# Optimization experiments

Measured on AMD Instinct MI355X. Metric: run time of the kernel, lower is better.

## Reference

```python
import jax, jax.numpy as jnp
import numpy as np

DIM = 4096
N_HEADS = 32
N_KV = 8
HD = 128
SW = 4096          # sliding window / cache length
B = 32             # max_batch_size (decode batch)
MAX_SEQ = 8192
START_POS = 4000
CURRENT_POS = 4000

def _nearest_32(n):
    return ((n + 31) // 32) * 32

PADDED_LEN = min(_nearest_32(START_POS + 1), SW)  # 4032

def _rope_tables():
    inv_freq = 1.0 / (10000.0 ** (np.arange(0, HD, 2, dtype=np.float32) / HD))
    t = np.arange(MAX_SEQ, dtype=np.float32)
    freqs = np.outer(t, inv_freq)                       # [MAX_SEQ, HD/2]
    emb = np.concatenate([freqs, freqs], axis=-1)       # [MAX_SEQ, HD]
    return jnp.asarray(np.cos(emb)), jnp.asarray(np.sin(emb))

def rotate_half(u):
    u1, u2 = jnp.split(u, 2, axis=-1)
    return jnp.concatenate([-u2, u1], axis=-1)

def setup_inputs() -> dict:
    key = jax.random.key(0)
    ks = jax.random.split(key, 6)
    cos_cached, sin_cached = _rope_tables()
    return {
        "x": jax.random.normal(ks[0], (1, 1, B, DIM), jnp.float32),
        "wqkv": jax.random.normal(ks[1], (DIM, DIM + 2 * N_KV * HD), jnp.float32) * 0.02,
        "wo": jax.random.normal(ks[2], (DIM, DIM), jnp.float32) * 0.02,
        "cache_k": jax.random.normal(ks[3], (B, N_KV, SW, HD), jnp.float32) * 0.5,
        "cache_v": jax.random.normal(ks[4], (B, N_KV, SW, HD), jnp.float32) * 0.5,
        "cos_cached": cos_cached,
        "sin_cached": sin_cached,
        "attn_mask": jnp.zeros((B, N_HEADS, 1, PADDED_LEN), jnp.float32),
        "start_pos": START_POS,
        "current_pos": CURRENT_POS,
    }

def reference(x, wqkv, wo, cache_k, cache_v, cos_cached, sin_cached, attn_mask,
              start_pos, current_pos):
    group = N_HEADS // N_KV
    padded_len = min(_nearest_32(start_pos + 1), SW)
    scale = 1.0 / jnp.sqrt(jnp.float32(HD))

    # fused QKV projection: x (1,1,B,DIM) @ wqkv -> (B, DIM + 2*N_KV*HD)
    xqkv = x[0, 0] @ wqkv
    q = xqkv[:, :DIM].reshape(B, N_HEADS, HD)
    k = xqkv[:, DIM:DIM + N_KV * HD].reshape(B, N_KV, HD)
    v = xqkv[:, DIM + N_KV * HD:].reshape(B, N_KV, HD)

    # rotary embedding at position start_pos (single decode token)
    cos = cos_cached[start_pos]   # [HD]
    sin = sin_cached[start_pos]
    q = q * cos + rotate_half(q) * sin
    k = k * cos + rotate_half(k) * sin

    # sliding-window KV cache update at current_pos
    cache_k = cache_k.at[:, :, current_pos, :].set(k)
    cache_v = cache_v.at[:, :, current_pos, :].set(v)
    keys = cache_k[:, :, :padded_len, :]     # [B, N_KV, L, HD]
    values = cache_v[:, :, :padded_len, :]

    # grouped attention: q heads grouped by kv head
    qg = q.reshape(B, N_KV, group, HD)
    scores = jnp.einsum('bkgd,bkld->bkgl', qg, keys) * scale
    scores = scores + attn_mask.reshape(B, N_KV, group, padded_len)
    probs = jax.nn.softmax(scores, axis=-1)
    out = jnp.einsum('bkgl,bkld->bkgd', probs, values)   # [B, N_KV, group, HD]

    # concat heads and output projection
    dense = out.reshape(B, DIM) @ wo
    return dense.reshape(1, 1, B, DIM)
```

## Files before the change

### kernel.cpp

```cpp
#include <hip/hip_runtime.h>
#include <hip/hip_bf16.h>

typedef unsigned int u32;
typedef unsigned short u16;

__device__ __forceinline__ u16 f2bf(float f){ u32 x; __builtin_memcpy(&x,&f,4); u32 r=(x+0x7fffu+((x>>16)&1u))>>16; return (u16)r; }
__device__ __forceinline__ float lo2f(u32 u){ u32 x=u<<16; float f; __builtin_memcpy(&f,&x,4); return f; }
__device__ __forceinline__ float hi2f(u32 u){ u32 x=u&0xffff0000u; float f; __builtin_memcpy(&f,&x,4); return f; }

__global__ __launch_bounds__(256) void transpose_x(
    const float* __restrict__ x, float* __restrict__ xt)
{
    __shared__ float ld[32][65];
    const int t = threadIdx.x;
    const int g = blockIdx.x;
    #pragma unroll
    for (int i=0;i<8;++i) {
        const int e = i*256 + t;
        const int b = e >> 6, dd = e & 63;
        ld[b][dd] = x[(size_t)b*4096 + g*64 + dd];
    }
    __syncthreads();
    #pragma unroll
    for (int i=0;i<8;++i) {
        const int e = i*256 + t;
        const int dd = e >> 5, b = e & 31;
        xt[(size_t)(g*64 + dd)*32 + b] = ld[b][dd];
    }
}

__global__ __launch_bounds__(256) void gemm_splitk_t(
    const float* __restrict__ At, const float2* __restrict__ W2,
    float* __restrict__ P, int K, int N, int dps)
{
    const int j2 = blockIdx.x*256 + threadIdx.x;
    const int s = blockIdx.y;
    float acc0[32], acc1[32];
    #pragma unroll
    for (int b=0;b<32;++b){ acc0[b]=0.f; acc1[b]=0.f; }
    const int d0 = s*dps, d1 = d0 + dps;
    const int halfN = N >> 1;
    #pragma unroll 2
    for (int d=d0; d<d1; ++d) {
        const float2 wv = W2[(size_t)d*halfN + j2];
        const float* __restrict__ Ad = At + d*32;
        #pragma unroll
        for (int b=0;b<32;++b) {
            const float av = Ad[b];
            acc0[b] = fmaf(av, wv.x, acc0[b]);
            acc1[b] = fmaf(av, wv.y, acc1[b]);
        }
    }
    float* Pp = P + (size_t)(s*32)*N + 2*j2;
    #pragma unroll
    for (int b=0;b<32;++b)
        *reinterpret_cast<float2*>(Pp + (size_t)b*N) = make_float2(acc0[b], acc1[b]);
}

__global__ __launch_bounds__(256) void qkv_finish(
    const float* __restrict__ P, const float* __restrict__ cosc,
    const float* __restrict__ sinc, const int* __restrict__ spp,
    float* __restrict__ qws, float* __restrict__ kn, float* __restrict__ vn,
    int splits)
{
    __shared__ float sh[256];
    const int t = threadIdx.x;
    const int col = blockIdx.x*256 + t;
    const int b = blockIdx.y;
    float v = 0.f;
    for (int s=0;s<splits;++s) v += P[(size_t)(s*32+b)*6144 + col];
    sh[t] = v;
    __syncthreads();
    if (col < 5120) {
        const int d = col & 127;
        const int pt = (t & ~127) | ((d<64)? d+64 : d-64);
        const float pv = sh[pt];
        const int spos = *spp;
        const float c  = cosc[spos*128 + d];
        const float sn = sinc[spos*128 + d];
        const float rot = (d<64)? -pv : pv;
        const float val = fmaf(v, c, rot*sn);
        if (col < 4096) qws[(size_t)b*4096 + col] = val;
        else            kn[(size_t)b*1024 + (col-4096)] = val;
    } else {
        vn[(size_t)b*1024 + (col-5120)] = v;
    }
}

__global__ __launch_bounds__(1024, 4) void attn_kernel(
    const float* __restrict__ qws, const float* __restrict__ Kc,
    const float* __restrict__ Vc, const float* __restrict__ kn,
    const float* __restrict__ vn, const float* __restrict__ mask,
    const int* __restrict__ curp, float* __restrict__ aout_t,
    const int PL, const int SW)
{
    __shared__ float scoresS[4*4100];
    __shared__ uint2 probsP[4096];
    __shared__ float obuf[16][4][128];
    __shared__ float redm[16][4];
    __shared__ float reds[16][4];

    const int t = threadIdx.x;
    const int lane = t & 63;
    const int w = t >> 6;
    const int b  = blockIdx.x >> 3;
    const int kv = blockIdx.x & 7;
    const int cur = *curp;

    const size_t mat = (size_t)(b*8+kv);
    const float* __restrict__ Kb  = Kc + mat*(size_t)SW*128;
    const float* __restrict__ knr = kn + mat*128;
    const float* __restrict__ qbase = qws + (size_t)(b*32 + kv*4)*128;

    const int l   = lane & 15;
    const int grp = lane >> 4;
    float qv[4][8];
    #pragma unroll
    for (int h=0;h<4;++h)
        #pragma unroll
        for (int j=0;j<8;++j)
            qv[h][j] = qbase[h*128 + l*8 + j];

    const int rpw = PL >> 4;
    const int rb0 = w * rpw;
    for (int g=0; g<rpw; g+=4) {
        const int r = rb0 + g + grp;
        const float* __restrict__ row = (r==cur) ? knr : (Kb + (size_t)r*128);
        const float4 ka = *reinterpret_cast<const float4*>(row + l*8);
        const float4 kb4 = *reinterpret_cast<const float4*>(row + l*8 + 4);
        float kf[8];
        kf[0]=ka.x; kf[1]=ka.y; kf[2]=ka.z; kf[3]=ka.w;
        kf[4]=kb4.x; kf[5]=kb4.y; kf[6]=kb4.z; kf[7]=kb4.w;
        float sc0=0.f, sc1=0.f, sc2=0.f, sc3=0.f;
        #pragma unroll
        for (int j=0;j<8;++j) {
            sc0 = fmaf(qv[0][j], kf[j], sc0);
            sc1 = fmaf(qv[1][j], kf[j], sc1);
            sc2 = fmaf(qv[2][j], kf[j], sc2);
            sc3 = fmaf(qv[3][j], kf[j], sc3);
        }
        #pragma unroll
        for (int off=8; off; off>>=1) {
            sc0 += __shfl_xor(sc0, off, 16);
            sc1 += __shfl_xor(sc1, off, 16);
            sc2 += __shfl_xor(sc2, off, 16);
            sc3 += __shfl_xor(sc3, off, 16);
        }
        if (l < 4) {
            const float v = (l==0)?sc0:(l==1)?sc1:(l==2)?sc2:sc3;
            scoresS[l*4100 + r] = v;
        }
    }
    __syncthreads();

    const float scale = 0.08838834764831845f;
    const size_t mbase = ((size_t)b*32 + (size_t)kv*4)*(size_t)PL;
    float s[4][4];
    #pragma unroll
    for (int i=0;i<4;++i) {
        const int p = i*1024 + t;
        if (p < PL) {
            #pragma unroll
            for (int h=0;h<4;++h) {
                const float mv = mask[mbase + (size_t)h*PL + p];
                s[h][i] = fmaf(scoresS[h*4100 + p], scale, mv);
            }
        } else {
            #pragma unroll
            for (int h=0;h<4;++h) s[h][i] = -3.0e38f;
        }
    }

    float lm[4];
    #pragma unroll
    for (int h=0;h<4;++h)
        lm[h] = fmaxf(fmaxf(s[h][0],s[h][1]), fmaxf(s[h][2],s[h][3]));
    #pragma unroll
    for (int off=1; off<64; off<<=1) {
        #pragma unroll
        for (int h=0;h<4;++h) lm[h] = fmaxf(lm[h], __shfl_xor(lm[h], off, 64));
    }
    if (lane==0) {
        #pragma unroll
        for (int h=0;h<4;++h) redm[w][h] = lm[h];
    }
    __syncthreads();
    float M[4];
    #pragma unroll
    for (int h=0;h<4;++h) {
        float m = redm[0][h];
        #pragma unroll
        for (int ww=1;ww<16;++ww) m = fmaxf(m, redm[ww][h]);
        M[h] = m;
    }

    float ls[4] = {0.f,0.f,0.f,0.f};
    #pragma unroll
    for (int i=0;i<4;++i) {
        #pragma unroll
        for (int h=0;h<4;++h) {
            const float e = __expf(s[h][i] - M[h]);
            s[h][i] = e;
            ls[h] += e;
        }
    }
    #pragma unroll
    for (int off=1; off<64; off<<=1) {
        #pragma unroll
        for (int h=0;h<4;++h) ls[h] += __shfl_xor(ls[h], off, 64);
    }
    if (lane==0) {
        #pragma unroll
        for (int h=0;h<4;++h) reds[w][h] = ls[h];
    }
    __syncthreads();
    float inv[4];
    #pragma unroll
    for (int h=0;h<4;++h) {
        float sm = reds[0][h];
        #pragma unroll
        for (int ww=1;ww<16;++ww) sm += reds[ww][h];
        inv[h] = 1.f / sm;
    }

    #pragma unroll
    for (int i=0;i<4;++i) {
        const int p = i*1024 + t;
        if (p < PL) {
            const u32 plo = (u32)f2bf(s[0][i]*inv[0]) | ((u32)f2bf(s[1][i]*inv[1]) << 16);
            const u32 phi = (u32)f2bf(s[2][i]*inv[2]) | ((u32)f2bf(s[3][i]*inv[3]) << 16);
            probsP[p] = make_uint2(plo, phi);
        }
    }
    __syncthreads();

    const float* __restrict__ Vb  = Vc + mat*(size_t)SW*128;
    const float* __restrict__ vnr = vn + mat*128;
    const int chunk = PL >> 4;
    const int p0 = w*chunk, p1 = p0 + chunk;
    float a0[4] = {0.f,0.f,0.f,0.f}, a1[4] = {0.f,0.f,0.f,0.f};
    #pragma unroll 8
    for (int p=p0; p<p1; ++p) {
        const float* row = (p==cur) ? vnr : (Vb + (size_t)p*128);
        const float2 vv = *reinterpret_cast<const float2*>(row + 2*lane);
        const uint2 pp = probsP[p];
        const float pr0 = lo2f(pp.x), pr1 = hi2f(pp.x);
        const float pr2 = lo2f(pp.y), pr3 = hi2f(pp.y);
        a0[0]=fmaf(pr0,vv.x,a0[0]); a1[0]=fmaf(pr0,vv.y,a1[0]);
        a0[1]=fmaf(pr1,vv.x,a0[1]); a1[1]=fmaf(pr1,vv.y,a1[1]);
        a0[2]=fmaf(pr2,vv.x,a0[2]); a1[2]=fmaf(pr2,vv.y,a1[2]);
        a0[3]=fmaf(pr3,vv.x,a0[3]); a1[3]=fmaf(pr3,vv.y,a1[3]);
    }
    #pragma unroll
    for (int h=0;h<4;++h)
        *reinterpret_cast<float2*>(&obuf[w][h][2*lane]) = make_float2(a0[h], a1[h]);
    __syncthreads();

    if (t < 512) {
        const int h = t >> 7;
        const int d = t & 127;
        float sum = obuf[0][h][d];
        #pragma unroll
        for (int ww=1;ww<16;++ww) sum += obuf[ww][h][d];
        const int col = (kv*4 + h)*128 + d;
        aout_t[(size_t)col*32 + b] = sum;
    }
}

__global__ __launch_bounds__(256) void wo_finish(
    const float* __restrict__ P, float* __restrict__ out, int splits)
{
    const int col = blockIdx.x*256 + threadIdx.x;
    const int b = blockIdx.y;
    float v = 0.f;
    for (int s=0;s<splits;++s) v += P[(size_t)(s*32+b)*4096 + col];
    out[(size_t)b*4096 + col] = v;
}

extern "C" void kernel_launch(void* const* d_in, const int* in_sizes, int n_in,
                              void* d_out, int out_size, void* d_ws, size_t ws_size,
                              hipStream_t stream)
{
    const float* x    = (const float*)d_in[0];
    const float* wqkv = (const float*)d_in[1];
    const float* wo   = (const float*)d_in[2];
    const float* cK   = (const float*)d_in[3];
    const float* cV   = (const float*)d_in[4];
    const float* cosc = (const float*)d_in[5];
    const float* sinc = (const float*)d_in[6];
    const float* mask = (const float*)d_in[7];
    const int* sp   = (const int*)d_in[8];
    const int* cp   = (const int*)d_in[9];

    const int PL = in_sizes[7] / (32*32);
    const int SW = in_sizes[3] / (32*8*128);

    char* ws = (char*)d_ws;
    float* xt    = (float*)(ws);
    float* qws   = (float*)(ws + 524288);
    float* aout_t= (float*)(ws + 2*524288);
    float* kn    = (float*)(ws + 3*524288);
    float* vn    = (float*)(ws + 3*524288 + 131072);
    float* Pbuf  = (float*)(ws + 3*524288 + 2*131072);

    int splits = 64;
    {
        const size_t fixed = 3ull*524288 + 2ull*131072;
        while (splits > 4 && fixed + (size_t)splits*32*6144*4 > ws_size) splits >>= 1;
    }
    const int dps = 4096 / splits;

    transpose_x<<<64, 256, 0, stream>>>(x, xt);
    gemm_splitk_t<<<dim3(12, splits), 256, 0, stream>>>(xt, (const float2*)wqkv, Pbuf, 4096, 6144, dps);
    qkv_finish<<<dim3(24, 32), 256, 0, stream>>>(Pbuf, cosc, sinc, sp, qws, kn, vn, splits);

    attn_kernel<<<256, 1024, 0, stream>>>(qws, cK, cV, kn, vn, mask, cp, aout_t, PL, SW);

    gemm_splitk_t<<<dim3(8, splits), 256, 0, stream>>>(aout_t, (const float2*)wo, Pbuf, 4096, 4096, dps);
    wo_finish<<<dim3(16, 32), 256, 0, stream>>>(Pbuf, (float*)d_out, splits);
}
```

Measured before the change: 305.0 us.

## Split attention over sequence into partial blocks with flash-decoding combine

Replaces the one-block-per-(batch,kv-head) attention kernel with a split-sequence version: each (batch,kv) pair is split into 8 partitions run by 256-thread blocks that write partial outputs plus running max and sum, and a new combine kernel merges them with log-sum-exp rescaling. This raises the block count from 256 to 2048 to better fill the GPU and hide KV-cache load latency. It costs an extra launch and a round trip for the partial results, and the workspace layout assumes a fixed Pbuf size instead of checking ws_size. Probabilities are stored unnormalised in bf16 before the rescale.

```diff
diff --git a/kernel.cpp b/kernel.cpp
--- a/kernel.cpp
+++ b/kernel.cpp
@@ -87,29 +87,31 @@
     }
 }
 
-__global__ __launch_bounds__(1024, 4) void attn_kernel(
+__global__ __launch_bounds__(256, 8) void attn_part(
     const float* __restrict__ qws, const float* __restrict__ Kc,
     const float* __restrict__ Vc, const float* __restrict__ kn,
     const float* __restrict__ vn, const float* __restrict__ mask,
-    const int* __restrict__ curp, float* __restrict__ aout_t,
-    const int PL, const int SW)
-{
-    __shared__ float scoresS[4*4100];
-    __shared__ uint2 probsP[4096];
-    __shared__ float obuf[16][4][128];
-    __shared__ float redm[16][4];
-    __shared__ float reds[16][4];
+    const int* __restrict__ curp, float* __restrict__ partO,
+    float* __restrict__ partML, const int PL, const int SW)
+{
+    __shared__ float scoresS[4*512];
+    __shared__ float obuf[4][4][128];
+    __shared__ float redm[4][4];
+    __shared__ float reds[4][4];
 
     const int t = threadIdx.x;
     const int lane = t & 63;
     const int w = t >> 6;
-    const int b  = blockIdx.x >> 3;
-    const int kv = blockIdx.x & 7;
+    const int mat  = blockIdx.x >> 3;
+    const int part = blockIdx.x & 7;
+    const int b  = mat >> 3;
+    const int kv = mat & 7;
     const int cur = *curp;
-
-    const size_t mat = (size_t)(b*8+kv);
-    const float* __restrict__ Kb  = Kc + mat*(size_t)SW*128;
-    const float* __restrict__ knr = kn + mat*128;
+    const int PS = PL >> 3;
+    const int base = part * PS;
+
+    const float* __restrict__ Kb  = Kc + (size_t)mat*SW*128;
+    const float* __restrict__ knr = kn + (size_t)mat*128;
     const float* __restrict__ qbase = qws + (size_t)(b*32 + kv*4)*128;
 
     const int l   = lane & 15;
@@ -121,49 +123,52 @@
         for (int j=0;j<8;++j)
             qv[h][j] = qbase[h*128 + l*8 + j];
 
-    const int rpw = PL >> 4;
-    const int rb0 = w * rpw;
-    for (int g=0; g<rpw; g+=4) {
-        const int r = rb0 + g + grp;
-        const float* __restrict__ row = (r==cur) ? knr : (Kb + (size_t)r*128);
-        const float4 ka = *reinterpret_cast<const float4*>(row + l*8);
-        const float4 kb4 = *reinterpret_cast<const float4*>(row + l*8 + 4);
-        float kf[8];
-        kf[0]=ka.x; kf[1]=ka.y; kf[2]=ka.z; kf[3]=ka.w;
-        kf[4]=kb4.x; kf[5]=kb4.y; kf[6]=kb4.z; kf[7]=kb4.w;
-        float sc0=0.f, sc1=0.f, sc2=0.f, sc3=0.f;
-        #pragma unroll
-        for (int j=0;j<8;++j) {
-            sc0 = fmaf(qv[0][j], kf[j], sc0);
-            sc1 = fmaf(qv[1][j], kf[j], sc1);
-            sc2 = fmaf(qv[2][j], kf[j], sc2);
-            sc3 = fmaf(qv[3][j], kf[j], sc3);
-        }
-        #pragma unroll
-        for (int off=8; off; off>>=1) {
-            sc0 += __shfl_xor(sc0, off, 16);
-            sc1 += __shfl_xor(sc1, off, 16);
-            sc2 += __shfl_xor(sc2, off, 16);
-            sc3 += __shfl_xor(sc3, off, 16);
-        }
-        if (l < 4) {
-            const float v = (l==0)?sc0:(l==1)?sc1:(l==2)?sc2:sc3;
-            scoresS[l*4100 + r] = v;
+    const int nIter = (PS + 15) >> 4;
+    for (int i=0;i<nIter;++i) {
+        const int rl = i*16 + w*4 + grp;
+        if (rl < PS) {
+            const int r = base + rl;
+            const float* __restrict__ row = (r==cur) ? knr : (Kb + (size_t)r*128);
+            const float4 ka  = *reinterpret_cast<const float4*>(row + l*8);
+            const float4 kb4 = *reinterpret_cast<const float4*>(row + l*8 + 4);
+            float kf[8];
+            kf[0]=ka.x; kf[1]=ka.y; kf[2]=ka.z; kf[3]=ka.w;
+            kf[4]=kb4.x; kf[5]=kb4.y; kf[6]=kb4.z; kf[7]=kb4.w;
+            float sc0=0.f, sc1=0.f, sc2=0.f, sc3=0.f;
+            #pragma unroll
+            for (int j=0;j<8;++j) {
+                sc0 = fmaf(qv[0][j], kf[j], sc0);
+                sc1 = fmaf(qv[1][j], kf[j], sc1);
+                sc2 = fmaf(qv[2][j], kf[j], sc2);
+                sc3 = fmaf(qv[3][j], kf[j], sc3);
+            }
+            #pragma unroll
+            for (int off=8; off; off>>=1) {
+                sc0 += __shfl_xor(sc0, off, 16);
+                sc1 += __shfl_xor(sc1, off, 16);
+                sc2 += __shfl_xor(sc2, off, 16);
+                sc3 += __shfl_xor(sc3, off, 16);
+            }
+            if (l < 4) {
+                const float v = (l==0)?sc0:(l==1)?sc1:(l==2)?sc2:sc3;
+                scoresS[l*512 + rl] = v;
+            }
         }
     }
     __syncthreads();
 
     const float scale = 0.08838834764831845f;
     const size_t mbase = ((size_t)b*32 + (size_t)kv*4)*(size_t)PL;
-    float s[4][4];
-    #pragma unroll
-    for (int i=0;i<4;++i) {
-        const int p = i*1024 + t;
-        if (p < PL) {
+    float s[4][2];
+    #pragma unroll
+    for (int i=0;i<2;++i) {
+        const int p = i*256 + t;
+        if (p < PS) {
+            const int gp = base + p;
             #pragma unroll
             for (int h=0;h<4;++h) {
-                const float mv = mask[mbase + (size_t)h*PL + p];
-                s[h][i] = fmaf(scoresS[h*4100 + p], scale, mv);
+                const float mv = mask[mbase + (size_t)h*PL + gp];
+                s[h][i] = fmaf(scoresS[h*512 + p], scale, mv);
             }
         } else {
             #pragma unroll
@@ -173,30 +178,25 @@
 
     float lm[4];
     #pragma unroll
+    for (int h=0;h<4;++h) lm[h] = fmaxf(s[h][0], s[h][1]);
+    #pragma unroll
+    for (int off=1; off<64; off<<=1) {
+        #pragma unroll
+        for (int h=0;h<4;++h) lm[h] = fmaxf(lm[h], __shfl_xor(lm[h], off, 64));
+    }
+    if (lane==0) {
+        #pragma unroll
+        for (int h=0;h<4;++h) redm[w][h] = lm[h];
+    }
+    __syncthreads();
+    float M[4];
+    #pragma unroll
     for (int h=0;h<4;++h)
-        lm[h] = fmaxf(fmaxf(s[h][0],s[h][1]), fmaxf(s[h][2],s[h][3]));
-    #pragma unroll
-    for (int off=1; off<64; off<<=1) {
-        #pragma unroll
-        for (int h=0;h<4;++h) lm[h] = fmaxf(lm[h], __shfl_xor(lm[h], off, 64));
-    }
-    if (lane==0) {
-        #pragma unroll
-        for (int h=0;h<4;++h) redm[w][h] = lm[h];
-    }
-    __syncthreads();
-    float M[4];
-    #pragma unroll
-    for (int h=0;h<4;++h) {
-        float m = redm[0][h];
-        #pragma unroll
-        for (int ww=1;ww<16;++ww) m = fmaxf(m, redm[ww][h]);
-        M[h] = m;
-    }
+        M[h] = fmaxf(fmaxf(redm[0][h],redm[1][h]), fmaxf(redm[2][h],redm[3][h]));
 
     float ls[4] = {0.f,0.f,0.f,0.f};
     #pragma unroll
-    for (int i=0;i<4;++i) {
+    for (int i=0;i<2;++i) {
         #pragma unroll
         for (int h=0;h<4;++h) {
             const float e = __expf(s[h][i] - M[h]);
@@ -214,38 +214,37 @@
         for (int h=0;h<4;++h) reds[w][h] = ls[h];
     }
     __syncthreads();
-    float inv[4];
-    #pragma unroll
-    for (int h=0;h<4;++h) {
-        float sm = reds[0][h];
-        #pragma unroll
-        for (int ww=1;ww<16;++ww) sm += reds[ww][h];
-        inv[h] = 1.f / sm;
-    }
-
-    #pragma unroll
-    for (int i=0;i<4;++i) {
-        const int p = i*1024 + t;
-        if (p < PL) {
-            const u32 plo = (u32)f2bf(s[0][i]*inv[0]) | ((u32)f2bf(s[1][i]*inv[1]) << 16);
-            const u32 phi = (u32)f2bf(s[2][i]*inv[2]) | ((u32)f2bf(s[3][i]*inv[3]) << 16);
-            probsP[p] = make_uint2(plo, phi);
-        }
-    }
-    __syncthreads();
-
-    const float* __restrict__ Vb  = Vc + mat*(size_t)SW*128;
-    const float* __restrict__ vnr = vn + mat*128;
-    const int chunk = PL >> 4;
+    float lsum[4];
+    #pragma unroll
+    for (int h=0;h<4;++h)
+        lsum[h] = reds[0][h]+reds[1][h]+reds[2][h]+reds[3][h];
+
+    #pragma unroll
+    for (int i=0;i<2;++i) {
+        const int p = i*256 + t;
+        if (p < PS) {
+            const u32 plo = (u32)f2bf(s[0][i]) | ((u32)f2bf(s[1][i]) << 16);
+            const u32 phi = (u32)f2bf(s[2][i]) | ((u32)f2bf(s[3][i]) << 16);
+            *reinterpret_cast<u32*>(&scoresS[p])       = plo;
+            *reinterpret_cast<u32*>(&scoresS[512 + p]) = phi;
+        }
+    }
+    __syncthreads();
+
+    const float* __restrict__ Vb  = Vc + (size_t)mat*SW*128;
+    const float* __restrict__ vnr = vn + (size_t)mat*128;
+    const int chunk = PS >> 2;
     const int p0 = w*chunk, p1 = p0 + chunk;
     float a0[4] = {0.f,0.f,0.f,0.f}, a1[4] = {0.f,0.f,0.f,0.f};
-    #pragma unroll 8
+    #pragma unroll 4
     for (int p=p0; p<p1; ++p) {
-        const float* row = (p==cur) ? vnr : (Vb + (size_t)p*128);
+        const int gr = base + p;
+        const float* row = (gr==cur) ? vnr : (Vb + (size_t)gr*128);
         const float2 vv = *reinterpret_cast<const float2*>(row + 2*lane);
-        const uint2 pp = probsP[p];
-        const float pr0 = lo2f(pp.x), pr1 = hi2f(pp.x);
-        const float pr2 = lo2f(pp.y), pr3 = hi2f(pp.y);
+        const u32 ppl = *reinterpret_cast<const u32*>(&scoresS[p]);
+        const u32 pph = *reinterpret_cast<const u32*>(&scoresS[512 + p]);
+        const float pr0 = lo2f(ppl), pr1 = hi2f(ppl);
+        const float pr2 = lo2f(pph), pr3 = hi2f(pph);
         a0[0]=fmaf(pr0,vv.x,a0[0]); a1[0]=fmaf(pr0,vv.y,a1[0]);
         a0[1]=fmaf(pr1,vv.x,a0[1]); a1[1]=fmaf(pr1,vv.y,a1[1]);
         a0[2]=fmaf(pr2,vv.x,a0[2]); a1[2]=fmaf(pr2,vv.y,a1[2]);
@@ -256,15 +255,45 @@
         *reinterpret_cast<float2*>(&obuf[w][h][2*lane]) = make_float2(a0[h], a1[h]);
     __syncthreads();
 
-    if (t < 512) {
-        const int h = t >> 7;
-        const int d = t & 127;
-        float sum = obuf[0][h][d];
-        #pragma unroll
-        for (int ww=1;ww<16;++ww) sum += obuf[ww][h][d];
-        const int col = (kv*4 + h)*128 + d;
-        aout_t[(size_t)col*32 + b] = sum;
-    }
+    #pragma unroll
+    for (int rr=0; rr<2; ++rr) {
+        const int idx = rr*256 + t;
+        const int h = idx >> 7;
+        const int d = idx & 127;
+        const float sum = obuf[0][h][d]+obuf[1][h][d]+obuf[2][h][d]+obuf[3][h][d];
+        partO[(size_t)blockIdx.x*512 + idx] = sum;
+    }
+    if (t < 4) {
+        partML[(size_t)blockIdx.x*8 + t]     = M[t];
+        partML[(size_t)blockIdx.x*8 + 4 + t] = lsum[t];
+    }
+}
+
+__global__ __launch_bounds__(512) void attn_combine(
+    const float* __restrict__ partO, const float* __restrict__ partML,
+    float* __restrict__ aout_t)
+{
+    const int mat = blockIdx.x;
+    const int t = threadIdx.x;
+    const int h = t >> 7, d = t & 127;
+    float m_[8], l_[8];
+    float M = -3.0e38f;
+    #pragma unroll
+    for (int p=0;p<8;++p) {
+        m_[p] = partML[(size_t)(mat*8+p)*8 + h];
+        l_[p] = partML[(size_t)(mat*8+p)*8 + 4 + h];
+        M = fmaxf(M, m_[p]);
+    }
+    float num = 0.f, den = 0.f;
+    #pragma unroll
+    for (int p=0;p<8;++p) {
+        const float sc = __expf(m_[p] - M);
+        num = fmaf(sc, partO[(size_t)(mat*8+p)*512 + t], num);
+        den = fmaf(sc, l_[p], den);
+    }
+    const int b = mat >> 3, kv = mat & 7;
+    const int col = (kv*4 + h)*128 + d;
+    aout_t[(size_t)col*32 + b] = num/den;
 }
 
 __global__ __launch_bounds__(256) void wo_finish(
@@ -302,11 +331,14 @@
     float* kn    = (float*)(ws + 3*524288);
     float* vn    = (float*)(ws + 3*524288 + 131072);
     float* Pbuf  = (float*)(ws + 3*524288 + 2*131072);
+    float* partO = (float*)(ws + 3*524288 + 2*131072 + 50331648);
+    float* partML= (float*)(ws + 3*524288 + 2*131072 + 50331648 + 4194304);
 
     int splits = 64;
     {
-        const size_t fixed = 3ull*524288 + 2ull*131072;
-        while (splits > 4 && fixed + (size_t)splits*32*6144*4 > ws_size) splits >>= 1;
+        const size_t fixed = 3ull*524288 + 2ull*131072 + 50331648ull + 4194304ull + 65536ull;
+        while (splits > 4 && (size_t)splits*32*6144*4 > 50331648ull) splits >>= 1;
+        (void)fixed;
     }
     const int dps = 4096 / splits;
 
@@ -314,7 +346,8 @@
     gemm_splitk_t<<<dim3(12, splits), 256, 0, stream>>>(xt, (const float2*)wqkv, Pbuf, 4096, 6144, dps);
     qkv_finish<<<dim3(24, 32), 256, 0, stream>>>(Pbuf, cosc, sinc, sp, qws, kn, vn, splits);
 
-    attn_kernel<<<256, 1024, 0, stream>>>(qws, cK, cV, kn, vn, mask, cp, aout_t, PL, SW);
+    attn_part<<<2048, 256, 0, stream>>>(qws, cK, cV, kn, vn, mask, cp, partO, partML, PL, SW);
+    attn_combine<<<256, 512, 0, stream>>>(partO, partML, aout_t);
 
     gemm_splitk_t<<<dim3(8, splits), 256, 0, stream>>>(aout_t, (const float2*)wo, Pbuf, 4096, 4096, dps);
     wo_finish<<<dim3(16, 32), 256, 0, stream>>>(Pbuf, (float*)d_out, splits);
```

After: 318.1 us. 1.04x slower.
